# Performance work log

Hardware: AMD Instinct MI355X
Metric: run time of the kernel (lower is better)

Reference implementation:

```python
import jax, jax.numpy as jnp
import numpy as np

B, S, D, H = 4, 2048, 1024, 16
HD = D // H  # head_dim = 64


def setup_inputs() -> dict:
    key = jax.random.key(0)
    ks = jax.random.split(key, 5)
    scale = 1.0 / np.sqrt(D)
    return {
        "x": jax.random.normal(ks[0], (B, S, D), dtype=jnp.float32),
        "Wq": jax.random.normal(ks[1], (D, D), dtype=jnp.float32) * scale,
        "bq": jnp.zeros((D,), dtype=jnp.float32),
        "Wk": jax.random.normal(ks[2], (D, D), dtype=jnp.float32) * scale,
        "bk": jnp.zeros((D,), dtype=jnp.float32),
        "Wv": jax.random.normal(ks[3], (D, D), dtype=jnp.float32) * scale,
        "bv": jnp.zeros((D,), dtype=jnp.float32),
        "Wp": jax.random.normal(ks[4], (D, D), dtype=jnp.float32) * scale,
        "bp": jnp.zeros((D,), dtype=jnp.float32),
    }


def reference(x, Wq, bq, Wk, bk, Wv, bv, Wp, bp):
    b, s, d = x.shape
    # qkv projections (torch Linear: x @ W.T + b; here W stored as (in,out))
    q = (x @ Wq + bq).reshape(b, s, H, HD).transpose(0, 2, 1, 3)  # (b,h,s,hd)
    k = (x @ Wk + bk).reshape(b, s, H, HD).transpose(0, 2, 1, 3)
    v = (x @ Wv + bv).reshape(b, s, H, HD).transpose(0, 2, 1, 3)
    scores = jnp.einsum("bhqd,bhkd->bhqk", q, k) / np.sqrt(HD)
    causal = jnp.tril(jnp.ones((s, s), dtype=bool))
    scores = jnp.where(causal, scores, -jnp.inf)
    attn = jax.nn.softmax(scores, axis=-1)  # dropout is identity (p=0 / eval)
    out = jnp.einsum("bhqk,bhkd->bhqd", attn, v)
    out = out.transpose(0, 2, 1, 3).reshape(b, s, d)
    return out @ Wp + bp
```

## Files before the change

### kernel.cpp

```cpp
#include <hip/hip_runtime.h>

typedef __bf16 bf16;
typedef __attribute__((ext_vector_type(4))) __bf16 bf16x4;
typedef __attribute__((ext_vector_type(8))) __bf16 bf16x8;
typedef __attribute__((ext_vector_type(4))) float f32x4;
typedef __attribute__((ext_vector_type(4))) unsigned int u32x4;

#define B_ 4
#define S_ 2048
#define D_ 1024
#define H_ 16
#define HD_ 64

#define GLB(p) ((const __attribute__((address_space(1))) void*)(p))
#define LDS(p) ((__attribute__((address_space(3))) void*)(p))

__global__ __launch_bounds__(256) void transpose_cvt(
    const float* __restrict__ W0, const float* __restrict__ W1,
    const float* __restrict__ W2, const float* __restrict__ W3,
    bf16* __restrict__ T0, bf16* __restrict__ T1,
    bf16* __restrict__ T2, bf16* __restrict__ T3)
{
    __shared__ float tile[32][33];
    int z = blockIdx.z;
    const float* W = (z == 0) ? W0 : (z == 1) ? W1 : (z == 2) ? W2 : W3;
    bf16*        T = (z == 0) ? T0 : (z == 1) ? T1 : (z == 2) ? T2 : T3;
    int bx = blockIdx.x * 32, by = blockIdx.y * 32;
    int tx = threadIdx.x & 31, ty = threadIdx.x >> 5;
    #pragma unroll
    for (int j = 0; j < 32; j += 8)
        tile[ty + j][tx] = W[(size_t)(by + ty + j) * D_ + bx + tx];
    __syncthreads();
    #pragma unroll
    for (int j = 0; j < 32; j += 8)
        T[(size_t)(bx + ty + j) * D_ + by + tx] = (bf16)tile[tx][ty + j];
}

__global__ __launch_bounds__(256) void cvt_x(
    const float* __restrict__ X, bf16* __restrict__ Xb)
{
    size_t i = ((size_t)blockIdx.x * 256 + threadIdx.x) * 8;
    f32x4 a = *(const f32x4*)(X + i);
    f32x4 b = *(const f32x4*)(X + i + 4);
    bf16x8 v;
    #pragma unroll
    for (int j = 0; j < 4; ++j) { v[j] = (bf16)a[j]; v[4 + j] = (bf16)b[j]; }
    *(bf16x8*)(Xb + i) = v;
}

__global__ __launch_bounds__(256) void qkv_gemm(
    const bf16* __restrict__ Xb,
    const bf16* __restrict__ WqT, const bf16* __restrict__ WkT, const bf16* __restrict__ WvT,
    const float* __restrict__ bq, const float* __restrict__ bk, const float* __restrict__ bv,
    bf16* __restrict__ Qo, bf16* __restrict__ Ko, bf16* __restrict__ Vo)
{
    const int z = blockIdx.z;
    const bf16*  WT   = (z == 0) ? WqT : (z == 1) ? WkT : WvT;
    const float* bias = (z == 0) ? bq  : (z == 1) ? bk  : bv;
    bf16*        out  = (z == 0) ? Qo  : (z == 1) ? Ko  : Vo;
    const float scale = (z == 0) ? 0.18033688011112042f : 1.0f;

    __shared__ bf16 As[128 * 32];
    __shared__ bf16 Bs[128 * 32];

    const int t = threadIdx.x;
    const int lid = t & 63, w = t >> 6;
    const int wm = w & 1, wn = w >> 1;
    const int lrow = lid & 15, quad = lid >> 4;
    const int m0 = blockIdx.y * 128, n0 = blockIdx.x * 128;

    const bf16* Ag = Xb + (size_t)m0 * D_;
    const bf16* Bg = WT + (size_t)n0 * D_;

    const int row0 = t >> 2, k80 = (t & 3) << 3;
    const int row1 = (t + 256) >> 2;

    f32x4 acc[4][4] = {};

    for (int k0 = 0; k0 < D_; k0 += 32) {
        __syncthreads();
        __builtin_amdgcn_global_load_lds(GLB(Ag + (size_t)row0 * D_ + k0 + k80),
                                         LDS(As + t * 8), 16, 0, 0);
        __builtin_amdgcn_global_load_lds(GLB(Bg + (size_t)row0 * D_ + k0 + k80),
                                         LDS(Bs + t * 8), 16, 0, 0);
        __builtin_amdgcn_global_load_lds(GLB(Ag + (size_t)row1 * D_ + k0 + k80),
                                         LDS(As + t * 8 + 2048), 16, 0, 0);
        __builtin_amdgcn_global_load_lds(GLB(Bg + (size_t)row1 * D_ + k0 + k80),
                                         LDS(Bs + t * 8 + 2048), 16, 0, 0);
        __syncthreads();
        bf16x8 a[4], b[4];
        #pragma unroll
        for (int mb = 0; mb < 4; ++mb)
            a[mb] = *(const bf16x8*)(As + (wm * 64 + mb * 16 + lrow) * 32 + quad * 8);
        #pragma unroll
        for (int nb = 0; nb < 4; ++nb)
            b[nb] = *(const bf16x8*)(Bs + (wn * 64 + nb * 16 + lrow) * 32 + quad * 8);
        #pragma unroll
        for (int mb = 0; mb < 4; ++mb)
            #pragma unroll
            for (int nb = 0; nb < 4; ++nb)
                acc[mb][nb] = __builtin_amdgcn_mfma_f32_16x16x32_bf16(a[mb], b[nb], acc[mb][nb], 0, 0, 0);
    }

    #pragma unroll
    for (int mb = 0; mb < 4; ++mb) {
        #pragma unroll
        for (int nb = 0; nb < 4; ++nb) {
            int gn = n0 + wn * 64 + nb * 16 + lrow;
            float bsv = bias[gn];
            int h = gn >> 6, hd = gn & 63;
            int gm0 = m0 + wm * 64 + mb * 16 + quad * 4;
            int bb = gm0 >> 11, s0 = gm0 & 2047;
            if (z == 2) {
                bf16x4 pk;
                #pragma unroll
                for (int r = 0; r < 4; ++r)
                    pk[r] = (bf16)(acc[mb][nb][r] + bsv);
                *(bf16x4*)(out + (((size_t)(bb * H_ + h)) * HD_ + hd) * S_ + s0) = pk;
            } else {
                #pragma unroll
                for (int r = 0; r < 4; ++r) {
                    float v = (acc[mb][nb][r] + bsv) * scale;
                    out[(((size_t)(bb * H_ + h)) * S_ + (s0 + r)) * HD_ + hd] = (bf16)v;
                }
            }
        }
    }
}

__global__ __launch_bounds__(256) void attn_fwd(
    const bf16* __restrict__ Q, const bf16* __restrict__ K,
    const bf16* __restrict__ Vt, bf16* __restrict__ O)
{
    __shared__ bf16 Ks[64 * 72];
    __shared__ bf16 Vs[64 * 72];
    __shared__ bf16 Ps[4 * 16 * 72];

    const int bh = blockIdx.y;
    const int t = threadIdx.x, lid = t & 63, w = t >> 6;
    const int lrow = lid & 15, quad = lid >> 4;
    const int b = bh >> 4, h = bh & 15;

    #pragma unroll 1
    for (int half = 0; half < 2; ++half) {
        const int qtile = half ? blockIdx.x : (31 - blockIdx.x);
        const int qbase = qtile * 64;

        const bf16* Qp = Q + ((size_t)bh * S_ + qbase + w * 16) * HD_;
        bf16x8 qf[2];
        #pragma unroll
        for (int ks = 0; ks < 2; ++ks)
            qf[ks] = *(const bf16x8*)(Qp + lrow * HD_ + ks * 32 + quad * 8);

        f32x4 o_acc[4] = {};
        float m_i = -3.0e4f, l_i = 0.0f;

        for (int kt = 0; kt <= qtile; ++kt) {
            const bf16* Kp = K  + ((size_t)bh * S_ + kt * 64) * HD_;
            const bf16* Vp = Vt + ((size_t)bh * HD_) * S_ + kt * 64;
            __syncthreads();
            #pragma unroll
            for (int i = 0; i < 2; ++i) {
                int c = t + i * 256;
                int row = c >> 3, c8 = (c & 7) << 3;
                *(u32x4*)(Ks + row * 72 + c8) = *(const u32x4*)(Kp + (size_t)row * HD_ + c8);
                *(u32x4*)(Vs + row * 72 + c8) = *(const u32x4*)(Vp + (size_t)row * S_ + c8);
            }
            __syncthreads();

            f32x4 sa[4] = {};
            #pragma unroll
            for (int ks = 0; ks < 2; ++ks) {
                #pragma unroll
                for (int nb = 0; nb < 4; ++nb) {
                    bf16x8 kf = *(const bf16x8*)(Ks + (nb * 16 + lrow) * 72 + ks * 32 + quad * 8);
                    sa[nb] = __builtin_amdgcn_mfma_f32_16x16x32_bf16(kf, qf[ks], sa[nb], 0, 0, 0);
                }
            }
            if (kt == qtile) {
                int q = qbase + w * 16 + lrow;
                #pragma unroll
                for (int nb = 0; nb < 4; ++nb) {
                    int key = kt * 64 + nb * 16 + quad * 4;
                    #pragma unroll
                    for (int r = 0; r < 4; ++r)
                        if (key + r > q) sa[nb][r] = -3.0e4f;
                }
            }

            float p[4][4];
            {
                float rm = sa[0][0];
                #pragma unroll
                for (int nb = 0; nb < 4; ++nb)
                    #pragma unroll
                    for (int r = 0; r < 4; ++r)
                        rm = fmaxf(rm, sa[nb][r]);
                rm = fmaxf(rm, __shfl_xor(rm, 16));
                rm = fmaxf(rm, __shfl_xor(rm, 32));
                float mnew = fmaxf(m_i, rm);
                float al = exp2f(m_i - mnew);
                m_i = mnew;
                float rs = 0.0f;
                #pragma unroll
                for (int nb = 0; nb < 4; ++nb)
                    #pragma unroll
                    for (int r = 0; r < 4; ++r) {
                        float e = exp2f(sa[nb][r] - mnew);
                        p[nb][r] = e;
                        rs += e;
                    }
                rs += __shfl_xor(rs, 16);
                rs += __shfl_xor(rs, 32);
                l_i = l_i * al + rs;
                #pragma unroll
                for (int nb = 0; nb < 4; ++nb)
                    #pragma unroll
                    for (int r = 0; r < 4; ++r)
                        o_acc[nb][r] *= al;
            }

            bf16* Pw = Ps + w * 16 * 72;
            #pragma unroll
            for (int nb = 0; nb < 4; ++nb) {
                bf16x4 pk;
                #pragma unroll
                for (int r = 0; r < 4; ++r)
                    pk[r] = (bf16)p[nb][r];
                *(bf16x4*)(Pw + lrow * 72 + nb * 16 + quad * 4) = pk;
            }
            asm volatile("s_waitcnt lgkmcnt(0)" ::: "memory");

            #pragma unroll
            for (int ks = 0; ks < 2; ++ks) {
                bf16x8 pf = *(const bf16x8*)(Pw + lrow * 72 + ks * 32 + quad * 8);
                #pragma unroll
                for (int nb = 0; nb < 4; ++nb) {
                    bf16x8 vf = *(const bf16x8*)(Vs + (nb * 16 + lrow) * 72 + ks * 32 + quad * 8);
                    o_acc[nb] = __builtin_amdgcn_mfma_f32_16x16x32_bf16(vf, pf, o_acc[nb], 0, 0, 0);
                }
            }
        }

        {
            float inv = 1.0f / l_i;
            int s = qbase + w * 16 + lrow;
            #pragma unroll
            for (int nb = 0; nb < 4; ++nb) {
                bf16x4 pk;
                #pragma unroll
                for (int r = 0; r < 4; ++r)
                    pk[r] = (bf16)(o_acc[nb][r] * inv);
                *(bf16x4*)(O + ((size_t)b * S_ + s) * D_ + h * 64 + nb * 16 + quad * 4) = pk;
            }
        }
        __syncthreads();
    }
}

__global__ __launch_bounds__(256) void proj_gemm(
    const bf16* __restrict__ A, const bf16* __restrict__ WpT,
    const float* __restrict__ bp, float* __restrict__ out)
{
    __shared__ bf16 As[128 * 32];
    __shared__ bf16 Bs[128 * 32];

    const int t = threadIdx.x;
    const int lid = t & 63, w = t >> 6;
    const int wm = w & 1, wn = w >> 1;
    const int lrow = lid & 15, quad = lid >> 4;
    const int m0 = blockIdx.y * 128, n0 = blockIdx.x * 128;

    const bf16* Ag = A   + (size_t)m0 * D_;
    const bf16* Bg = WpT + (size_t)n0 * D_;

    const int row0 = t >> 2, k80 = (t & 3) << 3;
    const int row1 = (t + 256) >> 2;

    f32x4 acc[4][4] = {};

    for (int k0 = 0; k0 < D_; k0 += 32) {
        __syncthreads();
        __builtin_amdgcn_global_load_lds(GLB(Ag + (size_t)row0 * D_ + k0 + k80),
                                         LDS(As + t * 8), 16, 0, 0);
        __builtin_amdgcn_global_load_lds(GLB(Bg + (size_t)row0 * D_ + k0 + k80),
                                         LDS(Bs + t * 8), 16, 0, 0);
        __builtin_amdgcn_global_load_lds(GLB(Ag + (size_t)row1 * D_ + k0 + k80),
                                         LDS(As + t * 8 + 2048), 16, 0, 0);
        __builtin_amdgcn_global_load_lds(GLB(Bg + (size_t)row1 * D_ + k0 + k80),
                                         LDS(Bs + t * 8 + 2048), 16, 0, 0);
        __syncthreads();
        bf16x8 a[4], b[4];
        #pragma unroll
        for (int mb = 0; mb < 4; ++mb)
            a[mb] = *(const bf16x8*)(As + (wm * 64 + mb * 16 + lrow) * 32 + quad * 8);
        #pragma unroll
        for (int nb = 0; nb < 4; ++nb)
            b[nb] = *(const bf16x8*)(Bs + (wn * 64 + nb * 16 + lrow) * 32 + quad * 8);
        #pragma unroll
        for (int mb = 0; mb < 4; ++mb)
            #pragma unroll
            for (int nb = 0; nb < 4; ++nb)
                acc[mb][nb] = __builtin_amdgcn_mfma_f32_16x16x32_bf16(a[mb], b[nb], acc[mb][nb], 0, 0, 0);
    }

    #pragma unroll
    for (int mb = 0; mb < 4; ++mb) {
        #pragma unroll
        for (int nb = 0; nb < 4; ++nb) {
            int gn = n0 + wn * 64 + nb * 16 + lrow;
            float bsv = bp[gn];
            #pragma unroll
            for (int r = 0; r < 4; ++r) {
                int gm = m0 + wm * 64 + mb * 16 + quad * 4 + r;
                out[(size_t)gm * D_ + gn] = acc[mb][nb][r] + bsv;
            }
        }
    }
}

extern "C" void kernel_launch(void* const* d_in, const int* in_sizes, int n_in,
                              void* d_out, int out_size, void* d_ws, size_t ws_size,
                              hipStream_t stream)
{
    const float* x  = (const float*)d_in[0];
    const float* Wq = (const float*)d_in[1];
    const float* bq = (const float*)d_in[2];
    const float* Wk = (const float*)d_in[3];
    const float* bk = (const float*)d_in[4];
    const float* Wv = (const float*)d_in[5];
    const float* bv = (const float*)d_in[6];
    const float* Wp = (const float*)d_in[7];
    const float* bp = (const float*)d_in[8];

    bf16* ws = (bf16*)d_ws;
    const size_t WSZ = (size_t)D_ * D_;
    const size_t BIG = (size_t)B_ * S_ * D_;
    bf16* WqT = ws;
    bf16* WkT = WqT + WSZ;
    bf16* WvT = WkT + WSZ;
    bf16* WpT = WvT + WSZ;
    bf16* Qb  = WpT + WSZ;
    bf16* Kb  = Qb + BIG;
    bf16* Vb  = Kb + BIG;
    bf16* Ab  = Vb + BIG;

    transpose_cvt<<<dim3(32, 32, 4), 256, 0, stream>>>(
        Wq, Wk, Wv, Wp, WqT, WkT, WvT, WpT);

    cvt_x<<<dim3(4096), 256, 0, stream>>>(x, Ab);

    qkv_gemm<<<dim3(8, 64, 3), 256, 0, stream>>>(
        Ab, WqT, WkT, WvT, bq, bk, bv, Qb, Kb, Vb);

    attn_fwd<<<dim3(16, 64), 256, 0, stream>>>(Qb, Kb, Vb, Ab);

    proj_gemm<<<dim3(8, 64), 256, 0, stream>>>(Ab, WpT, bp, (float*)d_out);
}
```

Baseline: 293.9 us.

## Double-buffer K/V tiles with direct global-to-LDS loads and XOR swizzle in attention

The attention kernel now double-buffers K and V tiles in LDS. The next tile is prefetched through global_load_lds while the current one is computed, so one barrier per iteration replaces two and load latency overlaps with MFMA work. The LDS layout switches from padded rows to an XOR swizzle to avoid bank conflicts, and MFMA sections run at raised wave priority. It also adds a lazy softmax rescale that skips the o_acc rescale when the running max grows by at most 8, trading some exp headroom for fewer multiplies and adding a wave-wide vote.

```diff
diff --git a/kernel.cpp b/kernel.cpp
--- a/kernel.cpp
+++ b/kernel.cpp
@@ -132,15 +132,24 @@
     const bf16* __restrict__ Q, const bf16* __restrict__ K,
     const bf16* __restrict__ Vt, bf16* __restrict__ O)
 {
-    __shared__ bf16 Ks[64 * 72];
-    __shared__ bf16 Vs[64 * 72];
-    __shared__ bf16 Ps[4 * 16 * 72];
+    __shared__ bf16 Ks[2][64 * 64];
+    __shared__ bf16 Vs[2][64 * 64];
+    __shared__ bf16 Ps[4][16 * 64];
 
     const int bh = blockIdx.y;
     const int t = threadIdx.x, lid = t & 63, w = t >> 6;
     const int lrow = lid & 15, quad = lid >> 4;
     const int b = bh >> 4, h = bh & 15;
 
+    const int swz = (lrow & 7) << 4;
+    const int rk0 = (quad * 16) ^ swz;
+    const int srow0 = t >> 3, srow1 = srow0 + 32;
+    const int sc = (t & 7) << 4;
+    const int kso0 = srow0 * 128 + (sc ^ ((srow0 & 7) << 4));
+    const int kso1 = srow1 * 128 + (sc ^ ((srow1 & 7) << 4));
+    const int vso0 = srow0 * (S_ * 2) + (sc ^ ((srow0 & 7) << 4));
+    const int vso1 = srow1 * (S_ * 2) + (sc ^ ((srow1 & 7) << 4));
+
     #pragma unroll 1
     for (int half = 0; half < 2; ++half) {
         const int qtile = half ? blockIdx.x : (31 - blockIdx.x);
@@ -155,28 +164,46 @@
         f32x4 o_acc[4] = {};
         float m_i = -3.0e4f, l_i = 0.0f;
 
+        const char* kp = (const char*)(K  + (size_t)bh * S_ * HD_);
+        const char* vp = (const char*)(Vt + (size_t)bh * HD_ * S_);
+
+        __builtin_amdgcn_global_load_lds(GLB(kp + kso0), LDS((char*)Ks[0] + t * 16), 16, 0, 0);
+        __builtin_amdgcn_global_load_lds(GLB(kp + kso1), LDS((char*)Ks[0] + t * 16 + 4096), 16, 0, 0);
+        __builtin_amdgcn_global_load_lds(GLB(vp + vso0), LDS((char*)Vs[0] + t * 16), 16, 0, 0);
+        __builtin_amdgcn_global_load_lds(GLB(vp + vso1), LDS((char*)Vs[0] + t * 16 + 4096), 16, 0, 0);
+        kp += 64 * HD_ * 2;
+        vp += 64 * 2;
+        asm volatile("s_waitcnt vmcnt(0)" ::: "memory");
+        __syncthreads();
+
+        int cur = 0;
         for (int kt = 0; kt <= qtile; ++kt) {
-            const bf16* Kp = K  + ((size_t)bh * S_ + kt * 64) * HD_;
-            const bf16* Vp = Vt + ((size_t)bh * HD_) * S_ + kt * 64;
-            __syncthreads();
-            #pragma unroll
-            for (int i = 0; i < 2; ++i) {
-                int c = t + i * 256;
-                int row = c >> 3, c8 = (c & 7) << 3;
-                *(u32x4*)(Ks + row * 72 + c8) = *(const u32x4*)(Kp + (size_t)row * HD_ + c8);
-                *(u32x4*)(Vs + row * 72 + c8) = *(const u32x4*)(Vp + (size_t)row * S_ + c8);
-            }
-            __syncthreads();
+            if (kt < qtile) {
+                char* kd = (char*)Ks[cur ^ 1] + t * 16;
+                char* vd = (char*)Vs[cur ^ 1] + t * 16;
+                __builtin_amdgcn_global_load_lds(GLB(kp + kso0), LDS(kd), 16, 0, 0);
+                __builtin_amdgcn_global_load_lds(GLB(kp + kso1), LDS(kd + 4096), 16, 0, 0);
+                __builtin_amdgcn_global_load_lds(GLB(vp + vso0), LDS(vd), 16, 0, 0);
+                __builtin_amdgcn_global_load_lds(GLB(vp + vso1), LDS(vd + 4096), 16, 0, 0);
+                kp += 8192; vp += 128;
+            }
+
+            const char* kb = (const char*)Ks[cur];
+            const char* vb = (const char*)Vs[cur];
 
             f32x4 sa[4] = {};
+            __builtin_amdgcn_s_setprio(1);
             #pragma unroll
             for (int ks = 0; ks < 2; ++ks) {
+                const int ro = rk0 ^ (ks * 64);
                 #pragma unroll
                 for (int nb = 0; nb < 4; ++nb) {
-                    bf16x8 kf = *(const bf16x8*)(Ks + (nb * 16 + lrow) * 72 + ks * 32 + quad * 8);
+                    bf16x8 kf = *(const bf16x8*)(kb + (nb * 16 + lrow) * 128 + ro);
                     sa[nb] = __builtin_amdgcn_mfma_f32_16x16x32_bf16(kf, qf[ks], sa[nb], 0, 0, 0);
                 }
             }
+            __builtin_amdgcn_s_setprio(0);
+
             if (kt == qtile) {
                 int q = qbase + w * 16 + lrow;
                 #pragma unroll
@@ -190,17 +217,15 @@
 
             float p[4][4];
             {
-                float rm = sa[0][0];
-                #pragma unroll
-                for (int nb = 0; nb < 4; ++nb)
-                    #pragma unroll
-                    for (int r = 0; r < 4; ++r)
-                        rm = fmaxf(rm, sa[nb][r]);
+                float rm = fmaxf(fmaxf(sa[0][0], sa[0][1]), fmaxf(sa[0][2], sa[0][3]));
+                #pragma unroll
+                for (int nb = 1; nb < 4; ++nb)
+                    rm = fmaxf(rm, fmaxf(fmaxf(sa[nb][0], sa[nb][1]),
+                                         fmaxf(sa[nb][2], sa[nb][3])));
                 rm = fmaxf(rm, __shfl_xor(rm, 16));
                 rm = fmaxf(rm, __shfl_xor(rm, 32));
-                float mnew = fmaxf(m_i, rm);
-                float al = exp2f(m_i - mnew);
-                m_i = mnew;
+                const bool heavy = !__all(rm <= m_i + 8.0f);
+                float mnew = heavy ? fmaxf(m_i, rm) : m_i;
                 float rs = 0.0f;
                 #pragma unroll
                 for (int nb = 0; nb < 4; ++nb)
@@ -212,34 +237,47 @@
                     }
                 rs += __shfl_xor(rs, 16);
                 rs += __shfl_xor(rs, 32);
-                l_i = l_i * al + rs;
-                #pragma unroll
-                for (int nb = 0; nb < 4; ++nb)
+                if (heavy) {
+                    float al = exp2f(m_i - mnew);
+                    m_i = mnew;
+                    l_i = l_i * al + rs;
                     #pragma unroll
-                    for (int r = 0; r < 4; ++r)
-                        o_acc[nb][r] *= al;
-            }
-
-            bf16* Pw = Ps + w * 16 * 72;
+                    for (int nb = 0; nb < 4; ++nb)
+                        #pragma unroll
+                        for (int r = 0; r < 4; ++r)
+                            o_acc[nb][r] *= al;
+                } else {
+                    l_i += rs;
+                }
+            }
+
+            char* pw = (char*)Ps[w] + lrow * 128;
             #pragma unroll
             for (int nb = 0; nb < 4; ++nb) {
                 bf16x4 pk;
                 #pragma unroll
                 for (int r = 0; r < 4; ++r)
                     pk[r] = (bf16)p[nb][r];
-                *(bf16x4*)(Pw + lrow * 72 + nb * 16 + quad * 4) = pk;
+                *(bf16x4*)(pw + ((nb * 32 + quad * 8) ^ swz)) = pk;
             }
             asm volatile("s_waitcnt lgkmcnt(0)" ::: "memory");
 
+            __builtin_amdgcn_s_setprio(1);
             #pragma unroll
             for (int ks = 0; ks < 2; ++ks) {
-                bf16x8 pf = *(const bf16x8*)(Pw + lrow * 72 + ks * 32 + quad * 8);
+                const int ro = rk0 ^ (ks * 64);
+                bf16x8 pf = *(const bf16x8*)(pw + ro);
                 #pragma unroll
                 for (int nb = 0; nb < 4; ++nb) {
-                    bf16x8 vf = *(const bf16x8*)(Vs + (nb * 16 + lrow) * 72 + ks * 32 + quad * 8);
+                    bf16x8 vf = *(const bf16x8*)(vb + (nb * 16 + lrow) * 128 + ro);
                     o_acc[nb] = __builtin_amdgcn_mfma_f32_16x16x32_bf16(vf, pf, o_acc[nb], 0, 0, 0);
                 }
             }
+            __builtin_amdgcn_s_setprio(0);
+
+            asm volatile("s_waitcnt vmcnt(0)" ::: "memory");
+            __syncthreads();
+            cur ^= 1;
         }
 
         {
@@ -254,7 +292,6 @@
                 *(bf16x4*)(O + ((size_t)b * S_ + s) * D_ + h * 64 + nb * 16 + quad * 4) = pk;
             }
         }
-        __syncthreads();
     }
 }
 
```

Result: slower. 304.7 us (+3.7%).

## Swizzle attention LDS, lazy softmax rescale, and MFMA row-sum

Applied to the files above, without the earlier changes.

Replaces the padded LDS layout for K, V and P tiles with an XOR-swizzled 128-byte-row layout to avoid bank conflicts without padding. Adds a wave-uniform lazy rescale that only updates the running max and rescales accumulators when the new max exceeds the old by more than a threshold. Computes the softmax denominator with an extra MFMA against a ones vector on the bf16 P values instead of shuffle reductions. It also switches to the fast hardware exp2 builtin and issues global loads before the LDS stores. The risks are a small numerical change, because the denominator is now summed from bf16-rounded P, and correctness that depends on the swizzle matching between writers and readers.

```diff
diff --git a/kernel.cpp b/kernel.cpp
--- a/kernel.cpp
+++ b/kernel.cpp
@@ -132,15 +132,29 @@
     const bf16* __restrict__ Q, const bf16* __restrict__ K,
     const bf16* __restrict__ Vt, bf16* __restrict__ O)
 {
-    __shared__ bf16 Ks[64 * 72];
-    __shared__ bf16 Vs[64 * 72];
-    __shared__ bf16 Ps[4 * 16 * 72];
+    __shared__ bf16 Ks[64 * 64];
+    __shared__ bf16 Vs[64 * 64];
+    __shared__ bf16 Ps[4][16 * 64];
 
     const int bh = blockIdx.y;
     const int t = threadIdx.x, lid = t & 63, w = t >> 6;
     const int lrow = lid & 15, quad = lid >> 4;
     const int b = bh >> 4, h = bh & 15;
 
+    const int swz = (lrow & 7) << 4;
+
+    const int srow0 = t >> 3, srow1 = srow0 + 32;
+    const int k8 = (t & 7) << 3;
+    const int sswz = ((t & 7) << 4) ^ ((srow0 & 7) << 4);
+    char* kdst0 = (char*)Ks + srow0 * 128 + sswz;
+    char* kdst1 = (char*)Ks + srow1 * 128 + sswz;
+    char* vdst0 = (char*)Vs + srow0 * 128 + sswz;
+    char* vdst1 = (char*)Vs + srow1 * 128 + sswz;
+
+    bf16x8 onesv;
+    #pragma unroll
+    for (int j = 0; j < 8; ++j) onesv[j] = (bf16)1.0f;
+
     #pragma unroll 1
     for (int half = 0; half < 2; ++half) {
         const int qtile = half ? blockIdx.x : (31 - blockIdx.x);
@@ -153,30 +167,34 @@
             qf[ks] = *(const bf16x8*)(Qp + lrow * HD_ + ks * 32 + quad * 8);
 
         f32x4 o_acc[4] = {};
-        float m_i = -3.0e4f, l_i = 0.0f;
+        f32x4 l_acc = {0.0f, 0.0f, 0.0f, 0.0f};
+        float m_i = -3.0e4f;
 
         for (int kt = 0; kt <= qtile; ++kt) {
             const bf16* Kp = K  + ((size_t)bh * S_ + kt * 64) * HD_;
             const bf16* Vp = Vt + ((size_t)bh * HD_) * S_ + kt * 64;
             __syncthreads();
-            #pragma unroll
-            for (int i = 0; i < 2; ++i) {
-                int c = t + i * 256;
-                int row = c >> 3, c8 = (c & 7) << 3;
-                *(u32x4*)(Ks + row * 72 + c8) = *(const u32x4*)(Kp + (size_t)row * HD_ + c8);
-                *(u32x4*)(Vs + row * 72 + c8) = *(const u32x4*)(Vp + (size_t)row * S_ + c8);
-            }
+            u32x4 kv0 = *(const u32x4*)(Kp + (size_t)srow0 * HD_ + k8);
+            u32x4 kv1 = *(const u32x4*)(Kp + (size_t)srow1 * HD_ + k8);
+            u32x4 vv0 = *(const u32x4*)(Vp + (size_t)srow0 * S_ + k8);
+            u32x4 vv1 = *(const u32x4*)(Vp + (size_t)srow1 * S_ + k8);
+            *(u32x4*)kdst0 = kv0;
+            *(u32x4*)kdst1 = kv1;
+            *(u32x4*)vdst0 = vv0;
+            *(u32x4*)vdst1 = vv1;
             __syncthreads();
 
             f32x4 sa[4] = {};
             #pragma unroll
             for (int ks = 0; ks < 2; ++ks) {
+                const int ro = ((ks << 6) + (quad << 4)) ^ swz;
                 #pragma unroll
                 for (int nb = 0; nb < 4; ++nb) {
-                    bf16x8 kf = *(const bf16x8*)(Ks + (nb * 16 + lrow) * 72 + ks * 32 + quad * 8);
+                    bf16x8 kf = *(const bf16x8*)((const char*)Ks + (nb * 16 + lrow) * 128 + ro);
                     sa[nb] = __builtin_amdgcn_mfma_f32_16x16x32_bf16(kf, qf[ks], sa[nb], 0, 0, 0);
                 }
             }
+
             if (kt == qtile) {
                 int q = qbase + w * 16 + lrow;
                 #pragma unroll
@@ -190,60 +208,62 @@
 
             float p[4][4];
             {
-                float rm = sa[0][0];
+                float r0 = fmaxf(fmaxf(sa[0][0], sa[0][1]), sa[0][2]);
+                float r1 = fmaxf(fmaxf(sa[0][3], sa[1][0]), sa[1][1]);
+                float r2 = fmaxf(fmaxf(sa[1][2], sa[1][3]), sa[2][0]);
+                float r3 = fmaxf(fmaxf(sa[2][1], sa[2][2]), sa[2][3]);
+                float r4 = fmaxf(fmaxf(sa[3][0], sa[3][1]), sa[3][2]);
+                float rm = fmaxf(fmaxf(fmaxf(r0, r1), r2),
+                                 fmaxf(fmaxf(r3, r4), sa[3][3]));
+                rm = fmaxf(rm, __shfl_xor(rm, 16));
+                rm = fmaxf(rm, __shfl_xor(rm, 32));
+                const bool heavy = !__all(rm <= m_i + 8.0f);
+                if (heavy) {
+                    float mnew = fmaxf(m_i, rm);
+                    float al = __builtin_amdgcn_exp2f(m_i - mnew);
+                    m_i = mnew;
+                    #pragma unroll
+                    for (int nb = 0; nb < 4; ++nb)
+                        #pragma unroll
+                        for (int r = 0; r < 4; ++r)
+                            o_acc[nb][r] *= al;
+                    #pragma unroll
+                    for (int r = 0; r < 4; ++r)
+                        l_acc[r] *= al;
+                }
                 #pragma unroll
                 for (int nb = 0; nb < 4; ++nb)
                     #pragma unroll
                     for (int r = 0; r < 4; ++r)
-                        rm = fmaxf(rm, sa[nb][r]);
-                rm = fmaxf(rm, __shfl_xor(rm, 16));
-                rm = fmaxf(rm, __shfl_xor(rm, 32));
-                float mnew = fmaxf(m_i, rm);
-                float al = exp2f(m_i - mnew);
-                m_i = mnew;
-                float rs = 0.0f;
-                #pragma unroll
-                for (int nb = 0; nb < 4; ++nb)
-                    #pragma unroll
-                    for (int r = 0; r < 4; ++r) {
-                        float e = exp2f(sa[nb][r] - mnew);
-                        p[nb][r] = e;
-                        rs += e;
-                    }
-                rs += __shfl_xor(rs, 16);
-                rs += __shfl_xor(rs, 32);
-                l_i = l_i * al + rs;
-                #pragma unroll
-                for (int nb = 0; nb < 4; ++nb)
-                    #pragma unroll
-                    for (int r = 0; r < 4; ++r)
-                        o_acc[nb][r] *= al;
-            }
-
-            bf16* Pw = Ps + w * 16 * 72;
+                        p[nb][r] = __builtin_amdgcn_exp2f(sa[nb][r] - m_i);
+            }
+
+            char* pw = (char*)Ps[w] + lrow * 128;
             #pragma unroll
             for (int nb = 0; nb < 4; ++nb) {
                 bf16x4 pk;
                 #pragma unroll
                 for (int r = 0; r < 4; ++r)
                     pk[r] = (bf16)p[nb][r];
-                *(bf16x4*)(Pw + lrow * 72 + nb * 16 + quad * 4) = pk;
+                *(bf16x4*)(pw + ((nb * 32 + quad * 8) ^ swz)) = pk;
             }
             asm volatile("s_waitcnt lgkmcnt(0)" ::: "memory");
 
             #pragma unroll
             for (int ks = 0; ks < 2; ++ks) {
-                bf16x8 pf = *(const bf16x8*)(Pw + lrow * 72 + ks * 32 + quad * 8);
+                const int ro = ((ks << 6) + (quad << 4)) ^ swz;
+                bf16x8 pf = *(const bf16x8*)(pw + ro);
                 #pragma unroll
                 for (int nb = 0; nb < 4; ++nb) {
-                    bf16x8 vf = *(const bf16x8*)(Vs + (nb * 16 + lrow) * 72 + ks * 32 + quad * 8);
+                    bf16x8 vf = *(const bf16x8*)((const char*)Vs + (nb * 16 + lrow) * 128 + ro);
                     o_acc[nb] = __builtin_amdgcn_mfma_f32_16x16x32_bf16(vf, pf, o_acc[nb], 0, 0, 0);
                 }
+                l_acc = __builtin_amdgcn_mfma_f32_16x16x32_bf16(onesv, pf, l_acc, 0, 0, 0);
             }
         }
 
         {
-            float inv = 1.0f / l_i;
+            float inv = 1.0f / l_acc[0];
             int s = qbase + w * 16 + lrow;
             #pragma unroll
             for (int nb = 0; nb < 4; ++nb) {
```

New measurement: 274.0 us. 1.07x faster.
